# Performance work log

Hardware: AMD Instinct MI355X
Metric: run time of the kernel (lower is better)

## Reference

```python
import jax, jax.numpy as jnp
import numpy as np
import math

HEADS = 4
DK = 64            # dim // heads
TEMP = 1.0
LMAX = 2048        # max segment length (for padded ragged attention)


def setup_inputs() -> dict:
    key = jax.random.key(0)
    ks = jax.random.split(key, 6)
    T, H, B = 1024, 256, 16
    # ragged lengths alternating 2048/1024 -> N = 24576
    lengths = np.tile(np.array([2048, 1024], dtype=np.int64), B // 2)
    N = int(lengths.sum())
    s = 1.0 / math.sqrt(H)
    return {
        "go_mat": jax.random.normal(ks[0], (T, H), jnp.float32),
        "node_h": jax.random.normal(ks[1], (N, H), jnp.float32),
        "Wq": jax.random.normal(ks[2], (H, H), jnp.float32) * s,
        "Wk": jax.random.normal(ks[3], (H, H), jnp.float32) * s,
        "Wv": jax.random.normal(ks[4], (H, H), jnp.float32) * s,
        "Wproj": jax.random.normal(ks[5], (H, H), jnp.float32) * s,
        "num_nodes_per_graph": jnp.asarray(lengths),
    }


def reference(go_mat, node_h, Wq, Wk, Wv, Wproj, num_nodes_per_graph):
    lengths = num_nodes_per_graph
    B = lengths.shape[0]
    N, H = node_h.shape
    T = go_mat.shape[0]

    # segment bookkeeping: graph id and within-graph offset for each node
    cum = jnp.cumsum(lengths)                       # [B]
    starts = cum - lengths                          # [B]
    g = jnp.searchsorted(cum, jnp.arange(N), side="right")  # [N] graph id
    off = jnp.arange(N) - starts[g]                 # [N] position within graph

    # projections (torch Linear: x @ W.T)
    Q = (go_mat @ Wq.T).reshape(T, HEADS, DK).transpose(1, 0, 2)   # [h,T,dk]
    K = node_h @ Wk.T                                              # [N,H]
    V = node_h @ Wv.T

    # scatter packed nodes into padded [B, Lmax, H]
    Kp = jnp.zeros((B, LMAX, H), K.dtype).at[g, off].set(K)
    Vp = jnp.zeros((B, LMAX, H), V.dtype).at[g, off].set(V)
    Kp = Kp.reshape(B, LMAX, HEADS, DK).transpose(0, 2, 1, 3)      # [B,h,L,dk]
    Vp = Vp.reshape(B, LMAX, HEADS, DK).transpose(0, 2, 1, 3)

    scores = jnp.einsum("htd,bhld->bhtl", Q, Kp) / (math.sqrt(DK) * TEMP)
    valid = jnp.arange(LMAX)[None, :] < lengths[:, None]           # [B,L]
    scores = jnp.where(valid[:, None, None, :], scores, jnp.float32(-1e30))
    attn = jax.nn.softmax(scores, axis=-1)                         # [B,h,T,L]

    ctx = jnp.einsum("bhtl,bhld->bhtd", attn, Vp)                  # [B,h,T,dk]
    ctx = ctx.transpose(0, 2, 1, 3).reshape(B, T, H)               # [B,T,H]
    return ctx @ Wproj.T
```

## Files before the change

kernel.cpp:

```cpp
#include <hip/hip_runtime.h>
#include <math.h>

#define HEADS 4
#define DK 64
#define HD 256

typedef __attribute__((ext_vector_type(8))) __bf16 bf16x8;
typedef __attribute__((ext_vector_type(4))) float floatx4;

__device__ __forceinline__ ushort f2bf(float f) {
  union { float f; unsigned u; } x; x.f = f;
  return (ushort)((x.u + 0x7FFF + ((x.u >> 16) & 1)) >> 16);
}

#if __has_builtin(__builtin_amdgcn_exp2f)
#define EXP2(x) __builtin_amdgcn_exp2f(x)
#else
#define EXP2(x) exp2f(x)
#endif

__device__ __forceinline__ unsigned pack_bf2(float lo, float hi) {
  union { float f; unsigned u; } a, b;
  a.f = lo; b.f = hi;
  return __builtin_amdgcn_perm(b.u + 0x8000u, a.u + 0x8000u, 0x07060302u);
}

#define GLDS(g, l) __builtin_amdgcn_global_load_lds(                      \
    (const __attribute__((address_space(1))) unsigned*)(g),               \
    (__attribute__((address_space(3))) unsigned*)(l), 16, 0, 0)

__global__ __launch_bounds__(256) void cvt_fused(
    const float* __restrict__ go, const float* __restrict__ nh,
    const float* __restrict__ w0, const float* __restrict__ w1,
    const float* __restrict__ w2, const float* __restrict__ w3,
    ushort* __restrict__ gobf, ushort* __restrict__ nodebf,
    ushort* __restrict__ wbf, int T, int N) {
  const int idx = blockIdx.x * 256 + threadIdx.x;
  const int row = idx >> 5, gr = idx & 31;
  if (row >= T + N + 4 * 256) return;
  const float* x; ushort* y; int r = row;
  if (row < T) { x = go; y = gobf; }
  else if (row < T + N) { x = nh; y = nodebf; r = row - T; }
  else {
    const int wr = row - T - N, wi = wr >> 8;
    r = wr & 255;
    x = (wi == 0) ? w0 : (wi == 1) ? w1 : (wi == 2) ? w2 : w3;
    y = wbf + (size_t)wi * HD * HD;
  }
  const int chunk = gr >> 3, g = gr & 7;
  const float* src = x + (size_t)r * 256 + gr * 8;
  float4 a = *(const float4*)src;
  float4 bq = *(const float4*)(src + 4);
  ushort* dst = y + (size_t)r * 256 + chunk * 64 + (g ^ (r & 7)) * 8;
  ushort4 o0 = {f2bf(a.x), f2bf(a.y), f2bf(a.z), f2bf(a.w)};
  ushort4 o1 = {f2bf(bq.x), f2bf(bq.y), f2bf(bq.z), f2bf(bq.w)};
  *(ushort4*)dst = o0;
  *(ushort4*)(dst + 4) = o1;
}

__device__ __forceinline__ void gemm_tile(const ushort* __restrict__ A,
                                          const ushort* __restrict__ W,
                                          ushort* __restrict__ C, int m0,
                                          int n0, int mode, int ldc,
                                          ushort* As, ushort* Ws, int lane,
                                          int w, int quad, int l15) {
  const int wm = w & 1, wn = w >> 1;
  floatx4 acc[4][2];
#pragma unroll
  for (int mt = 0; mt < 4; ++mt)
#pragma unroll
    for (int nt = 0; nt < 2; ++nt) acc[mt][nt] = (floatx4){0.f, 0.f, 0.f, 0.f};

  for (int k0 = 0; k0 < 256; k0 += 64) {
    __syncthreads();
#pragma unroll
    for (int t = 0; t < 4; ++t)
      GLDS(A + (size_t)(m0 + w * 32 + t * 8 + (lane >> 3)) * 256 + k0 + (lane & 7) * 8,
           &As[(w * 32 + t * 8) * 64]);
#pragma unroll
    for (int t = 0; t < 2; ++t)
      GLDS(W + (size_t)(n0 + w * 16 + t * 8 + (lane >> 3)) * 256 + k0 + (lane & 7) * 8,
           &Ws[(w * 16 + t * 8) * 64]);
    __syncthreads();

    bf16x8 af[4][2], bfr[2][2];
#pragma unroll
    for (int kk = 0; kk < 2; ++kk) {
      const int pg = ((kk * 4 + quad) ^ (l15 & 7)) * 8;
#pragma unroll
      for (int mt = 0; mt < 4; ++mt)
        af[mt][kk] = *(const bf16x8*)&As[(wm * 64 + mt * 16 + l15) * 64 + pg];
#pragma unroll
      for (int nt = 0; nt < 2; ++nt)
        bfr[nt][kk] = *(const bf16x8*)&Ws[(wn * 32 + nt * 16 + l15) * 64 + pg];
    }
#pragma unroll
    for (int kk = 0; kk < 2; ++kk)
#pragma unroll
      for (int mt = 0; mt < 4; ++mt)
#pragma unroll
        for (int nt = 0; nt < 2; ++nt)
          acc[mt][nt] = __builtin_amdgcn_mfma_f32_16x16x32_bf16(
              af[mt][kk], bfr[nt][kk], acc[mt][nt], 0, 0, 0);
  }

#pragma unroll
  for (int mt = 0; mt < 4; ++mt)
#pragma unroll
    for (int nt = 0; nt < 2; ++nt) {
      const int col = n0 + wn * 32 + nt * 16 + l15;
      if (mode == 2) {
        const int d = col & 63;
        const int g = mt * 2 + (quad >> 1);
        const int node = m0 + wm * 64 + (g ^ (d & 7)) * 8 + (quad & 1) * 4;
        ushort4 o = {f2bf(acc[mt][nt][0]), f2bf(acc[mt][nt][1]),
                     f2bf(acc[mt][nt][2]), f2bf(acc[mt][nt][3])};
        *(ushort4*)&C[(size_t)col * ldc + node] = o;
      } else {
#pragma unroll
        for (int r = 0; r < 4; ++r) {
          const int row = m0 + wm * 64 + mt * 16 + quad * 4 + r;
          if (mode == 3) {
            ((float*)C)[(size_t)row * 256 + col] = acc[mt][nt][r];
          } else {
            int cc = col;
            if (mode == 1)
              cc = (col & ~63) | (((((col >> 3) & 7) ^ (row & 7))) << 3) | (col & 7);
            C[(size_t)row * 256 + cc] = f2bf(acc[mt][nt][r]);
          }
        }
      }
    }
}

__global__ __launch_bounds__(256) void qkv_gemm(const ushort* __restrict__ gobf,
                                                const ushort* __restrict__ nodebf,
                                                const ushort* __restrict__ wbf,
                                                ushort* __restrict__ Qbf,
                                                ushort* __restrict__ Kgb,
                                                ushort* __restrict__ Vtb,
                                                int T, int N) {
  __shared__ __align__(16) ushort As[128 * 64];
  __shared__ __align__(16) ushort Ws[64 * 64];
  const int tid = threadIdx.x, lane = tid & 63, w = tid >> 6;
  const int quad = lane >> 4, l15 = lane & 15;
  const int QX = T >> 7, KB = N >> 7;
  const int NT = QX + 2 * KB;
  const int jx = blockIdx.x % NT;
  const int n0 = (blockIdx.x / NT) * 64;
  if (jx < QX)
    gemm_tile(gobf, wbf, Qbf, jx * 128, n0, 0, 0, As, Ws, lane, w, quad, l15);
  else if (jx < QX + KB)
    gemm_tile(nodebf, wbf + (size_t)HD * HD, Kgb, (jx - QX) * 128, n0, 1, 0,
              As, Ws, lane, w, quad, l15);
  else
    gemm_tile(nodebf, wbf + (size_t)2 * HD * HD, Vtb, (jx - QX - KB) * 128, n0,
              2, N, As, Ws, lane, w, quad, l15);
}

__global__ __launch_bounds__(256, 3) void attn_split(
    const ushort* __restrict__ Qb, const ushort* __restrict__ Kg,
    const ushort* __restrict__ Vt, const int* __restrict__ lens,
    float* __restrict__ Opart, float* __restrict__ Lpart,
    int T, int N, int B) {
  __shared__ __align__(16) ushort Ks[2][64 * 64];
  __shared__ __align__(16) ushort Vs[2][64 * 64];

  const int tid = threadIdx.x, lane = tid & 63, wave = tid >> 6;
  const int quad = lane >> 4, l15 = lane & 15;
  const int QX = T >> 7;
  const int nspl = N >> 10;
  const int grpc = HEADS * nspl;
  const int qx = blockIdx.x / grpc;
  const int rem = blockIdx.x - qx * grpc;
  const int h = rem / nspl;
  const int zid = rem - h * nspl;

  int z = zid, b, start = 0, len = 0, off = -1;
  for (b = 0; b < B; ++b) {
    len = lens[b];
    const int s = (len + 1023) >> 10;
    if (z < s) { off = z << 10; break; }
    z -= s; start += len;
  }
  if (off < 0) return;
  const int kcnt = min(1024, len - off);
  const int kbeg = start + off;

  const int q0 = qx * 128 + wave * 32;
  bf16x8 qb[2][2];
#pragma unroll
  for (int qt = 0; qt < 2; ++qt)
#pragma unroll
    for (int kk = 0; kk < 2; ++kk)
      qb[qt][kk] = *(const bf16x8*)(Qb + (size_t)(q0 + qt * 16 + l15) * 256 +
                                    h * 64 + kk * 32 + quad * 8);

  floatx4 o[2][4];
#pragma unroll
  for (int qt = 0; qt < 2; ++qt)
#pragma unroll
    for (int nt = 0; nt < 4; ++nt) o[qt][nt] = (floatx4){0.f, 0.f, 0.f, 0.f};
  float lsum[2] = {0.f, 0.f};

  const float sc = 0.18033688011112042f;
  const int srow = lane >> 3;
  const int scol = (lane & 7) * 8;

  GLDS(Kg + (size_t)(kbeg + wave * 8 + srow) * 256 + h * 64 + scol,
       &Ks[0][(wave * 8) * 64]);
  GLDS(Kg + (size_t)(kbeg + wave * 8 + 32 + srow) * 256 + h * 64 + scol,
       &Ks[0][(wave * 8 + 32) * 64]);
  GLDS(Vt + (size_t)(h * 64 + wave * 8 + srow) * (size_t)N + kbeg + scol,
       &Vs[0][(wave * 8) * 64]);
  GLDS(Vt + (size_t)(h * 64 + wave * 8 + 32 + srow) * (size_t)N + kbeg + scol,
       &Vs[0][(wave * 8 + 32) * 64]);

  int buf = 0;
  for (int j0 = 0; j0 < kcnt; j0 += 64, buf ^= 1) {
    __syncthreads();
    const int jn = j0 + 64;
    if (jn < kcnt) {
      GLDS(Kg + (size_t)(kbeg + jn + wave * 8 + srow) * 256 + h * 64 + scol,
           &Ks[buf ^ 1][(wave * 8) * 64]);
      GLDS(Kg + (size_t)(kbeg + jn + wave * 8 + 32 + srow) * 256 + h * 64 + scol,
           &Ks[buf ^ 1][(wave * 8 + 32) * 64]);
      GLDS(Vt + (size_t)(h * 64 + wave * 8 + srow) * (size_t)N + kbeg + jn + scol,
           &Vs[buf ^ 1][(wave * 8) * 64]);
      GLDS(Vt + (size_t)(h * 64 + wave * 8 + 32 + srow) * (size_t)N + kbeg + jn + scol,
           &Vs[buf ^ 1][(wave * 8 + 32) * 64]);
    }

    floatx4 st[4][2];
#pragma unroll
    for (int t = 0; t < 4; ++t)
#pragma unroll
      for (int qt = 0; qt < 2; ++qt) st[t][qt] = (floatx4){0.f, 0.f, 0.f, 0.f};
#pragma unroll
    for (int kk = 0; kk < 2; ++kk) {
#pragma unroll
      for (int t = 0; t < 4; ++t) {
        bf16x8 kf = *(const bf16x8*)&Ks[buf][(t * 16 + l15) * 64 +
                                            ((kk * 4 + quad) ^ (l15 & 7)) * 8];
        st[t][0] = __builtin_amdgcn_mfma_f32_16x16x32_bf16(kf, qb[0][kk], st[t][0], 0, 0, 0);
        st[t][1] = __builtin_amdgcn_mfma_f32_16x16x32_bf16(kf, qb[1][kk], st[t][1], 0, 0, 0);
      }
    }

    unsigned W[4][2][2];
    if (jn <= kcnt) {
#pragma unroll
      for (int t = 0; t < 4; ++t)
#pragma unroll
        for (int qt = 0; qt < 2; ++qt) {
          float p[4];
#pragma unroll
          for (int r = 0; r < 4; ++r) p[r] = EXP2(fmaf(st[t][qt][r], sc, -32.0f));
          lsum[qt] += (p[0] + p[1]) + (p[2] + p[3]);
          W[t][qt][0] = pack_bf2(p[0], p[1]);
          W[t][qt][1] = pack_bf2(p[2], p[3]);
        }
    } else {
#pragma unroll
      for (int t = 0; t < 4; ++t)
#pragma unroll
        for (int qt = 0; qt < 2; ++qt) {
          float p[4];
#pragma unroll
          for (int r = 0; r < 4; ++r) {
            const bool v = (j0 + t * 16 + quad * 4 + r) < kcnt;
            p[r] = v ? EXP2(fmaf(st[t][qt][r], sc, -32.0f)) : 0.0f;
          }
          lsum[qt] += (p[0] + p[1]) + (p[2] + p[3]);
          W[t][qt][0] = pack_bf2(p[0], p[1]);
          W[t][qt][1] = pack_bf2(p[2], p[3]);
        }
    }

#pragma unroll
    for (int ks = 0; ks < 2; ++ks) {
      bf16x8 pa[2];
#pragma unroll
      for (int qt = 0; qt < 2; ++qt) {
        unsigned a0 = W[2 * ks][qt][0], a1 = W[2 * ks][qt][1];
        unsigned b0 = W[2 * ks + 1][qt][0], b1 = W[2 * ks + 1][qt][1];
        asm("v_permlane32_swap_b32 %0, %1" : "+v"(a0), "+v"(b0));
        asm("v_permlane32_swap_b32 %0, %1" : "+v"(a1), "+v"(b1));
        asm("v_permlane16_swap_b32 %0, %1" : "+v"(a0), "+v"(b0));
        asm("v_permlane16_swap_b32 %0, %1" : "+v"(a1), "+v"(b1));
        union { uint4 u; bf16x8 v; } c;
        c.u = make_uint4(a0, a1, b0, b1);
        pa[qt] = c.v;
      }
#pragma unroll
      for (int nt = 0; nt < 4; ++nt) {
        bf16x8 vf = *(const bf16x8*)&Vs[buf][(nt * 16 + l15) * 64 +
                                            ((ks * 4 + quad) ^ (l15 & 7)) * 8];
        o[0][nt] = __builtin_amdgcn_mfma_f32_16x16x32_bf16(pa[0], vf, o[0][nt], 0, 0, 0);
        o[1][nt] = __builtin_amdgcn_mfma_f32_16x16x32_bf16(pa[1], vf, o[1][nt], 0, 0, 0);
      }
    }
  }

  const int part = (zid * HEADS + h) * QX + qx;
  float* op = Opart + (size_t)part * 8192;
#pragma unroll
  for (int qt = 0; qt < 2; ++qt) {
#pragma unroll
    for (int nt = 0; nt < 4; ++nt)
#pragma unroll
      for (int r = 0; r < 4; ++r)
        op[(wave * 32 + qt * 16 + quad * 4 + r) * 64 + nt * 16 + l15] = o[qt][nt][r];
    float lt = lsum[qt];
    lt += __shfl_xor(lt, 16);
    lt += __shfl_xor(lt, 32);
    if (lane < 16)
      Lpart[(size_t)part * 128 + wave * 32 + qt * 16 + lane] = lt;
  }
}

__global__ __launch_bounds__(256) void combine(const float* __restrict__ Opart,
                                               const float* __restrict__ Lpart,
                                               const int* __restrict__ lens,
                                               ushort* __restrict__ ctxb, int T) {
  const int t = threadIdx.x;
  const int row = blockIdx.x * 64 + (t >> 2);
  const int h = t & 3;
  const int b = row / T;
  const int tq = row - b * T;
  const int qx = tq >> 7, qr = tq & 127;
  const int QX = T >> 7;
  int z0 = 0;
  for (int i = 0; i < b; ++i) z0 += (lens[i] + 1023) >> 10;
  const int ns = (lens[b] + 1023) >> 10;

  float l = 0.f;
  float4 acc[16];
#pragma unroll
  for (int g = 0; g < 16; ++g) acc[g] = make_float4(0.f, 0.f, 0.f, 0.f);
  for (int s = 0; s < ns; ++s) {
    const size_t part = (size_t)((z0 + s) * HEADS + h) * QX + qx;
    l += Lpart[part * 128 + qr];
    const float4* src = (const float4*)(Opart + part * 8192 + (size_t)qr * 64);
#pragma unroll
    for (int g = 0; g < 16; ++g) {
      float4 v = src[g];
      acc[g].x += v.x; acc[g].y += v.y; acc[g].z += v.z; acc[g].w += v.w;
    }
  }
  const float inv = 1.0f / l;
  ushort* dst = ctxb + (size_t)row * 256 + h * 64;
#pragma unroll
  for (int gg = 0; gg < 8; ++gg) {
    const float4 a = acc[gg * 2], c = acc[gg * 2 + 1];
    const int phys = gg ^ (row & 7);
    ushort4 o0 = {f2bf(a.x * inv), f2bf(a.y * inv), f2bf(a.z * inv), f2bf(a.w * inv)};
    ushort4 o1 = {f2bf(c.x * inv), f2bf(c.y * inv), f2bf(c.z * inv), f2bf(c.w * inv)};
    *(ushort4*)&dst[phys * 8] = o0;
    *(ushort4*)&dst[phys * 8 + 4] = o1;
  }
}

__global__ __launch_bounds__(256) void proj_gemm(const ushort* __restrict__ ctxb,
                                                 const ushort* __restrict__ wbf,
                                                 float* __restrict__ outp) {
  __shared__ __align__(16) ushort As[128 * 64];
  __shared__ __align__(16) ushort Ws[64 * 64];
  const int tid = threadIdx.x, lane = tid & 63, w = tid >> 6;
  const int quad = lane >> 4, l15 = lane & 15;
  gemm_tile(ctxb, wbf + (size_t)3 * HD * HD, (ushort*)outp, blockIdx.x * 128,
            blockIdx.y * 64, 3, 0, As, Ws, lane, w, quad, l15);
}

extern "C" void kernel_launch(void* const* d_in, const int* in_sizes, int n_in,
                              void* d_out, int out_size, void* d_ws, size_t ws_size,
                              hipStream_t stream) {
  const float* go     = (const float*)d_in[0];
  const float* node_h = (const float*)d_in[1];
  const float* Wq     = (const float*)d_in[2];
  const float* Wk     = (const float*)d_in[3];
  const float* Wv     = (const float*)d_in[4];
  const float* Wproj  = (const float*)d_in[5];
  const int*   lens   = (const int*)d_in[6];

  const int T = in_sizes[0] / HD;
  const int N = in_sizes[1] / HD;
  const int B = in_sizes[6];
  const int NSPL = N >> 10;
  const int QX = T >> 7;
  const int KB = N >> 7;

  char* p = (char*)d_ws;
  ushort* Kgb  = (ushort*)p;  p += (size_t)N * HD * 2;
  ushort* Vtb  = (ushort*)p;  p += (size_t)N * HD * 2;
  ushort* Qbf  = (ushort*)p;  p += (size_t)T * HD * 2;
  ushort* gobf = (ushort*)p;  p += (size_t)T * HD * 2;
  ushort* ctxb = (ushort*)p;  p += (size_t)B * T * HD * 2;
  ushort* wbf  = (ushort*)p;  p += (size_t)4 * HD * HD * 2;
  ushort* nodebf = (ushort*)p;
  float* Opart = (float*)p;   p += (size_t)NSPL * HEADS * QX * 8192 * 4;
  float* Lpart = (float*)p;   p += (size_t)NSPL * HEADS * QX * 128 * 4;

  cvt_fused<<<((T + N + 1024) * 32 + 255) / 256, 256, 0, stream>>>(
      go, node_h, Wq, Wk, Wv, Wproj, gobf, nodebf, wbf, T, N);

  qkv_gemm<<<(QX + 2 * KB) * 4, 256, 0, stream>>>(gobf, nodebf, wbf, Qbf, Kgb,
                                                  Vtb, T, N);

  attn_split<<<QX * HEADS * NSPL, 256, 0, stream>>>(Qbf, Kgb, Vtb, lens,
                                                    Opart, Lpart, T, N, B);

  combine<<<(B * T) / 64, 256, 0, stream>>>(Opart, Lpart, lens, ctxb, T);

  proj_gemm<<<dim3((B * T) / 128, 4), 256, 0, stream>>>(ctxb, wbf, (float*)d_out);
}
```

Baseline: 156.4 us.

## Widen QKV GEMM tiles, add MFMA priority hints, use hardware bf16 pack

The QKV GEMM tile grows from 128x64 to 128x128 output columns through a templated gemm_tile, halving the grid and the re-reads of A tiles, at the cost of more accumulator registers and LDS. The attention kernel wraps its MFMA sections in s_setprio so matrix work gets issue priority over other waves. Probability packing switches from a manual perm-based rounding to the v_cvt_pk_bf16_f32 instruction, which may differ slightly in rounding. The conversion kernel now writes each 16-byte chunk with one store instead of two.

```diff
diff --git a/kernel.cpp b/kernel.cpp
--- a/kernel.cpp
+++ b/kernel.cpp
@@ -19,10 +19,10 @@
 #define EXP2(x) exp2f(x)
 #endif
 
-__device__ __forceinline__ unsigned pack_bf2(float lo, float hi) {
-  union { float f; unsigned u; } a, b;
-  a.f = lo; b.f = hi;
-  return __builtin_amdgcn_perm(b.u + 0x8000u, a.u + 0x8000u, 0x07060302u);
+__device__ __forceinline__ unsigned cvtpk_bf16(float lo, float hi) {
+  unsigned r;
+  asm("v_cvt_pk_bf16_f32 %0, %1, %2" : "=v"(r) : "v"(lo), "v"(hi));
+  return r;
 }
 
 #define GLDS(g, l) __builtin_amdgcn_global_load_lds(                      \
@@ -52,12 +52,13 @@
   float4 a = *(const float4*)src;
   float4 bq = *(const float4*)(src + 4);
   ushort* dst = y + (size_t)r * 256 + chunk * 64 + (g ^ (r & 7)) * 8;
-  ushort4 o0 = {f2bf(a.x), f2bf(a.y), f2bf(a.z), f2bf(a.w)};
-  ushort4 o1 = {f2bf(bq.x), f2bf(bq.y), f2bf(bq.z), f2bf(bq.w)};
-  *(ushort4*)dst = o0;
-  *(ushort4*)(dst + 4) = o1;
-}
-
+  union { ushort4 h[2]; uint4 q; } pk;
+  pk.h[0] = (ushort4){f2bf(a.x), f2bf(a.y), f2bf(a.z), f2bf(a.w)};
+  pk.h[1] = (ushort4){f2bf(bq.x), f2bf(bq.y), f2bf(bq.z), f2bf(bq.w)};
+  *(uint4*)dst = pk.q;
+}
+
+template <int NW>
 __device__ __forceinline__ void gemm_tile(const ushort* __restrict__ A,
                                           const ushort* __restrict__ W,
                                           ushort* __restrict__ C, int m0,
@@ -65,11 +66,11 @@
                                           ushort* As, ushort* Ws, int lane,
                                           int w, int quad, int l15) {
   const int wm = w & 1, wn = w >> 1;
-  floatx4 acc[4][2];
+  floatx4 acc[4][NW];
 #pragma unroll
   for (int mt = 0; mt < 4; ++mt)
 #pragma unroll
-    for (int nt = 0; nt < 2; ++nt) acc[mt][nt] = (floatx4){0.f, 0.f, 0.f, 0.f};
+    for (int nt = 0; nt < NW; ++nt) acc[mt][nt] = (floatx4){0.f, 0.f, 0.f, 0.f};
 
   for (int k0 = 0; k0 < 256; k0 += 64) {
     __syncthreads();
@@ -78,37 +79,35 @@
       GLDS(A + (size_t)(m0 + w * 32 + t * 8 + (lane >> 3)) * 256 + k0 + (lane & 7) * 8,
            &As[(w * 32 + t * 8) * 64]);
 #pragma unroll
-    for (int t = 0; t < 2; ++t)
-      GLDS(W + (size_t)(n0 + w * 16 + t * 8 + (lane >> 3)) * 256 + k0 + (lane & 7) * 8,
-           &Ws[(w * 16 + t * 8) * 64]);
+    for (int t = 0; t < NW; ++t)
+      GLDS(W + (size_t)(n0 + w * (8 * NW) + t * 8 + (lane >> 3)) * 256 + k0 + (lane & 7) * 8,
+           &Ws[(w * (8 * NW) + t * 8) * 64]);
     __syncthreads();
 
-    bf16x8 af[4][2], bfr[2][2];
 #pragma unroll
     for (int kk = 0; kk < 2; ++kk) {
       const int pg = ((kk * 4 + quad) ^ (l15 & 7)) * 8;
+      bf16x8 af[4], bfr[NW];
 #pragma unroll
       for (int mt = 0; mt < 4; ++mt)
-        af[mt][kk] = *(const bf16x8*)&As[(wm * 64 + mt * 16 + l15) * 64 + pg];
-#pragma unroll
-      for (int nt = 0; nt < 2; ++nt)
-        bfr[nt][kk] = *(const bf16x8*)&Ws[(wn * 32 + nt * 16 + l15) * 64 + pg];
-    }
-#pragma unroll
-    for (int kk = 0; kk < 2; ++kk)
+        af[mt] = *(const bf16x8*)&As[(wm * 64 + mt * 16 + l15) * 64 + pg];
+#pragma unroll
+      for (int nt = 0; nt < NW; ++nt)
+        bfr[nt] = *(const bf16x8*)&Ws[(wn * (16 * NW) + nt * 16 + l15) * 64 + pg];
 #pragma unroll
       for (int mt = 0; mt < 4; ++mt)
 #pragma unroll
-        for (int nt = 0; nt < 2; ++nt)
+        for (int nt = 0; nt < NW; ++nt)
           acc[mt][nt] = __builtin_amdgcn_mfma_f32_16x16x32_bf16(
-              af[mt][kk], bfr[nt][kk], acc[mt][nt], 0, 0, 0);
+              af[mt], bfr[nt], acc[mt][nt], 0, 0, 0);
+    }
   }
 
 #pragma unroll
   for (int mt = 0; mt < 4; ++mt)
 #pragma unroll
-    for (int nt = 0; nt < 2; ++nt) {
-      const int col = n0 + wn * 32 + nt * 16 + l15;
+    for (int nt = 0; nt < NW; ++nt) {
+      const int col = n0 + wn * (16 * NW) + nt * 16 + l15;
       if (mode == 2) {
         const int d = col & 63;
         const int g = mt * 2 + (quad >> 1);
@@ -141,21 +140,21 @@
                                                 ushort* __restrict__ Vtb,
                                                 int T, int N) {
   __shared__ __align__(16) ushort As[128 * 64];
-  __shared__ __align__(16) ushort Ws[64 * 64];
+  __shared__ __align__(16) ushort Ws[128 * 64];
   const int tid = threadIdx.x, lane = tid & 63, w = tid >> 6;
   const int quad = lane >> 4, l15 = lane & 15;
   const int QX = T >> 7, KB = N >> 7;
   const int NT = QX + 2 * KB;
   const int jx = blockIdx.x % NT;
-  const int n0 = (blockIdx.x / NT) * 64;
+  const int n0 = (blockIdx.x / NT) * 128;
   if (jx < QX)
-    gemm_tile(gobf, wbf, Qbf, jx * 128, n0, 0, 0, As, Ws, lane, w, quad, l15);
+    gemm_tile<4>(gobf, wbf, Qbf, jx * 128, n0, 0, 0, As, Ws, lane, w, quad, l15);
   else if (jx < QX + KB)
-    gemm_tile(nodebf, wbf + (size_t)HD * HD, Kgb, (jx - QX) * 128, n0, 1, 0,
-              As, Ws, lane, w, quad, l15);
+    gemm_tile<4>(nodebf, wbf + (size_t)HD * HD, Kgb, (jx - QX) * 128, n0, 1, 0,
+                 As, Ws, lane, w, quad, l15);
   else
-    gemm_tile(nodebf, wbf + (size_t)2 * HD * HD, Vtb, (jx - QX - KB) * 128, n0,
-              2, N, As, Ws, lane, w, quad, l15);
+    gemm_tile<4>(nodebf, wbf + (size_t)2 * HD * HD, Vtb, (jx - QX - KB) * 128,
+                 n0, 2, N, As, Ws, lane, w, quad, l15);
 }
 
 __global__ __launch_bounds__(256, 3) void attn_split(
@@ -236,6 +235,7 @@
     for (int t = 0; t < 4; ++t)
 #pragma unroll
       for (int qt = 0; qt < 2; ++qt) st[t][qt] = (floatx4){0.f, 0.f, 0.f, 0.f};
+    __builtin_amdgcn_s_setprio(1);
 #pragma unroll
     for (int kk = 0; kk < 2; ++kk) {
 #pragma unroll
@@ -246,6 +246,7 @@
         st[t][1] = __builtin_amdgcn_mfma_f32_16x16x32_bf16(kf, qb[1][kk], st[t][1], 0, 0, 0);
       }
     }
+    __builtin_amdgcn_s_setprio(0);
 
     unsigned W[4][2][2];
     if (jn <= kcnt) {
@@ -257,8 +258,8 @@
 #pragma unroll
           for (int r = 0; r < 4; ++r) p[r] = EXP2(fmaf(st[t][qt][r], sc, -32.0f));
           lsum[qt] += (p[0] + p[1]) + (p[2] + p[3]);
-          W[t][qt][0] = pack_bf2(p[0], p[1]);
-          W[t][qt][1] = pack_bf2(p[2], p[3]);
+          W[t][qt][0] = cvtpk_bf16(p[0], p[1]);
+          W[t][qt][1] = cvtpk_bf16(p[2], p[3]);
         }
     } else {
 #pragma unroll
@@ -272,8 +273,8 @@
             p[r] = v ? EXP2(fmaf(st[t][qt][r], sc, -32.0f)) : 0.0f;
           }
           lsum[qt] += (p[0] + p[1]) + (p[2] + p[3]);
-          W[t][qt][0] = pack_bf2(p[0], p[1]);
-          W[t][qt][1] = pack_bf2(p[2], p[3]);
+          W[t][qt][0] = cvtpk_bf16(p[0], p[1]);
+          W[t][qt][1] = cvtpk_bf16(p[2], p[3]);
         }
     }
 
@@ -292,6 +293,7 @@
         c.u = make_uint4(a0, a1, b0, b1);
         pa[qt] = c.v;
       }
+      __builtin_amdgcn_s_setprio(1);
 #pragma unroll
       for (int nt = 0; nt < 4; ++nt) {
         bf16x8 vf = *(const bf16x8*)&Vs[buf][(nt * 16 + l15) * 64 +
@@ -299,6 +301,7 @@
         o[0][nt] = __builtin_amdgcn_mfma_f32_16x16x32_bf16(pa[0], vf, o[0][nt], 0, 0, 0);
         o[1][nt] = __builtin_amdgcn_mfma_f32_16x16x32_bf16(pa[1], vf, o[1][nt], 0, 0, 0);
       }
+      __builtin_amdgcn_s_setprio(0);
     }
   }
 
@@ -368,8 +371,8 @@
   __shared__ __align__(16) ushort Ws[64 * 64];
   const int tid = threadIdx.x, lane = tid & 63, w = tid >> 6;
   const int quad = lane >> 4, l15 = lane & 15;
-  gemm_tile(ctxb, wbf + (size_t)3 * HD * HD, (ushort*)outp, blockIdx.x * 128,
-            blockIdx.y * 64, 3, 0, As, Ws, lane, w, quad, l15);
+  gemm_tile<2>(ctxb, wbf + (size_t)3 * HD * HD, (ushort*)outp, blockIdx.x * 128,
+               blockIdx.y * 64, 3, 0, As, Ws, lane, w, quad, l15);
 }
 
 extern "C" void kernel_launch(void* const* d_in, const int* in_sizes, int n_in,
@@ -404,7 +407,7 @@
   cvt_fused<<<((T + N + 1024) * 32 + 255) / 256, 256, 0, stream>>>(
       go, node_h, Wq, Wk, Wv, Wproj, gobf, nodebf, wbf, T, N);
 
-  qkv_gemm<<<(QX + 2 * KB) * 4, 256, 0, stream>>>(gobf, nodebf, wbf, Qbf, Kgb,
+  qkv_gemm<<<(QX + 2 * KB) * 2, 256, 0, stream>>>(gobf, nodebf, wbf, Qbf, Kgb,
                                                   Vtb, T, N);
 
   attn_split<<<QX * HEADS * NSPL, 256, 0, stream>>>(Qbf, Kgb, Vtb, lens,
```

Result: no change. 155.8 us (-0.4%).
